# Kernel tuning notes

Measured on AMD Instinct MI355X. Metric: run time of the kernel, lower is better.

The kernel has to match this reference:

```python
import jax, jax.numpy as jnp
import numpy as np

N, IN, OUT, R, E = 20000, 768, 768, 8, 320000


def setup_inputs() -> dict:
    key = jax.random.key(0)
    ks = jax.random.split(key, 9)
    x = jax.random.normal(ks[0], (N, IN), dtype=jnp.float32)
    edge_index = jax.random.randint(ks[1], (2, E), 0, N, dtype=jnp.int64)
    edge_type = jax.random.randint(ks[2], (E,), 0, R, dtype=jnp.int64)
    s1 = 1.0 / np.sqrt(IN)
    s2 = 1.0 / np.sqrt(OUT)
    W1 = jax.random.normal(ks[3], (R, IN, OUT), dtype=jnp.float32) * s1
    root1 = jax.random.normal(ks[4], (IN, OUT), dtype=jnp.float32) * s1
    b1 = jnp.zeros((OUT,), dtype=jnp.float32)
    W2 = jax.random.normal(ks[5], (R, OUT, OUT), dtype=jnp.float32) * s2
    root2 = jax.random.normal(ks[6], (OUT, OUT), dtype=jnp.float32) * s2
    b2 = jnp.zeros((OUT,), dtype=jnp.float32)
    return {"x": x, "edge_index": edge_index, "edge_type": edge_type,
            "W1": W1, "root1": root1, "b1": b1,
            "W2": W2, "root2": root2, "b2": b2}


def _rgcn_conv(x, src, dst, etype, W, root, b):
    # PyG RGCNConv: per-relation mean aggregation of neighbor features,
    # then relation-specific linear transform, plus root weight and bias.
    # mean(x_j @ W_r) == mean(x_j) @ W_r, so aggregate first, transform after.
    num_nodes = x.shape[0]
    num_rel = W.shape[0]
    x_src = x[src]                                  # [E, d_in]
    seg = dst * num_rel + etype                     # composite (node, relation) id
    sums = jax.ops.segment_sum(x_src, seg, num_segments=num_nodes * num_rel)
    cnt = jax.ops.segment_sum(jnp.ones((src.shape[0],), dtype=x.dtype), seg,
                              num_segments=num_nodes * num_rel)
    mean = sums / jnp.maximum(cnt, 1.0)[:, None]    # [N*R, d_in]
    mean = mean.reshape(num_nodes, num_rel, -1)     # [N, R, d_in]
    out = jnp.einsum('nri,rio->no', mean, W)        # relation-batched matmul
    return out + x @ root + b


def reference(x, edge_index, edge_type, W1, root1, b1, W2, root2, b2):
    src, dst = edge_index[0], edge_index[1]
    h = _rgcn_conv(x, src, dst, edge_type, W1, root1, b1)
    h = jax.nn.relu(h)
    out = _rgcn_conv(h, src, dst, edge_type, W2, root2, b2)
    return out
```

## Files before the change

### kernel.cpp

```cpp
#include <hip/hip_runtime.h>
#include <hip/hip_bf16.h>
#include <stdint.h>

#define N_NODES 20000
#define DIM     768
#define NREL    8
#define NEDGE   320000
#define NSEG    (N_NODES * NREL)
#define GKA     6144
#define GK      6912
#define NPW     2

typedef short short8 __attribute__((ext_vector_type(8)));
typedef float f32x4  __attribute__((ext_vector_type(4)));

__device__ __forceinline__ void async_load16(const void* g, void* l) {
  __builtin_amdgcn_global_load_lds((const __attribute__((address_space(1))) void*)g,
                                   (__attribute__((address_space(3))) void*)l,
                                   16, 0, 0);
}

__device__ __forceinline__ float bf_lo(uint32_t v) {
  return __builtin_bit_cast(float, v << 16);
}
__device__ __forceinline__ float bf_hi(uint32_t v) {
  return __builtin_bit_cast(float, v & 0xffff0000u);
}
__device__ __forceinline__ uint32_t pack_bf16x2(float a, float b) {
  uint32_t lo = __builtin_bit_cast(unsigned short, __float2bfloat16(a));
  uint32_t hi = __builtin_bit_cast(unsigned short, __float2bfloat16(b));
  return lo | (hi << 16);
}

__global__ void seg_count_kernel(const int* __restrict__ dst, const int* __restrict__ et,
                                 int* __restrict__ segcnt, int e_cnt) {
  int e = blockIdx.x * 256 + threadIdx.x;
  if (e < e_cnt) atomicAdd(&segcnt[dst[e] * NREL + et[e]], 1);
}

__global__ void block_scan_kernel(const int* __restrict__ in, int* __restrict__ out,
                                  int* __restrict__ partials, int n) {
  __shared__ int wsum[16];
  const int t = threadIdx.x, lane = t & 63, wave = t >> 6;
  const int i = blockIdx.x * 1024 + t;
  int v = (i < n) ? in[i] : 0;
  int s = v;
#pragma unroll
  for (int off = 1; off < 64; off <<= 1) {
    int u = __shfl_up(s, off, 64);
    if (lane >= off) s += u;
  }
  if (lane == 63) wsum[wave] = s;
  __syncthreads();
  if (t < 16) {
    int w = wsum[t];
#pragma unroll
    for (int off = 1; off < 16; off <<= 1) {
      int u = __shfl_up(w, off, 64);
      if (t >= off) w += u;
    }
    wsum[t] = w;
  }
  __syncthreads();
  const int basew = (wave > 0) ? wsum[wave - 1] : 0;
  if (i < n) out[i] = basew + s - v;
  if (t == 1023) partials[blockIdx.x] = wsum[15];
}

__global__ void partial_scan_kernel(int* __restrict__ partials, int nb) {
  const int lane = threadIdx.x & 63;
  int carry = 0;
  for (int base = 0; base < nb; base += 64) {
    const int i = base + lane;
    int v = (i < nb) ? partials[i] : 0;
    int s = v;
#pragma unroll
    for (int off = 1; off < 64; off <<= 1) {
      int u = __shfl_up(s, off, 64);
      if (lane >= off) s += u;
    }
    if (i < nb) partials[i] = carry + s - v;
    carry += __shfl(s, 63, 64);
  }
}

__global__ void add_offsets_kernel(int* __restrict__ soffs, const int* __restrict__ partials,
                                   int* __restrict__ cursor, int n) {
  const int i = blockIdx.x * 1024 + threadIdx.x;
  if (i < n) {
    const int v = soffs[i] + partials[blockIdx.x];
    soffs[i] = v;
    cursor[i] = v;
  }
  if (i == 0) soffs[n] = NEDGE;
}

__global__ void seg_scatter_kernel(const int* __restrict__ src, const int* __restrict__ dst,
                                   const int* __restrict__ et, int* __restrict__ cursor,
                                   int* __restrict__ es, int e_cnt) {
  int e = blockIdx.x * 256 + threadIdx.x;
  if (e < e_cnt) {
    const int seg = dst[e] * NREL + et[e];
    const int p = atomicAdd(&cursor[seg], 1);
    es[p] = src[e];
  }
}

__global__ void cvt_bf16_kernel(const float4* __restrict__ in, ushort4* __restrict__ out, int n4) {
  int i = blockIdx.x * 256 + threadIdx.x;
  if (i < n4) {
    float4 f = in[i];
    ushort4 r;
    r.x = __builtin_bit_cast(unsigned short, __float2bfloat16(f.x));
    r.y = __builtin_bit_cast(unsigned short, __float2bfloat16(f.y));
    r.z = __builtin_bit_cast(unsigned short, __float2bfloat16(f.z));
    r.w = __builtin_bit_cast(unsigned short, __float2bfloat16(f.w));
    out[i] = r;
  }
}

__global__ void transpose_w_kernel(const float* __restrict__ src, __hip_bfloat16* __restrict__ dst,
                                   int rows, int col_off) {
  __shared__ float tile[32][33];
  const int c0 = blockIdx.x * 32;
  const int r0 = blockIdx.y * 32;
  const int tx = threadIdx.x, ty = threadIdx.y;
  for (int i = ty; i < 32; i += 8) {
    int r = r0 + i, c = c0 + tx;
    tile[i][tx] = (r < rows) ? src[(size_t)r * DIM + c] : 0.f;
  }
  __syncthreads();
  for (int i = ty; i < 32; i += 8) {
    int c = c0 + i, r = r0 + tx;
    if (r < rows)
      dst[(size_t)c * GK + col_off + r] = __float2bfloat16(tile[tx][i]);
  }
}

__global__ __launch_bounds__(256) void aggregate_kernel(
    const __hip_bfloat16* __restrict__ feat,
    const int* __restrict__ soffs, const int* __restrict__ es,
    __hip_bfloat16* __restrict__ Abuf,
    int node_base, int rows) {
  const int t = threadIdx.x;
  const int lane = t & 63;
  const int wave = t >> 6;
  const int boff = lane * 8;

  int nloc = (blockIdx.x * 4 + wave) * NPW;
  for (int it = 0; it < NPW; ++it, ++nloc) {
    if (nloc >= rows) return;
    const int n = node_base + nloc;
    char* Ab = (char*)(Abuf + (size_t)nloc * GKA);
#pragma unroll
    for (int r = 0; r < NREL; ++r) {
      const int beg = soffs[n * NREL + r], end = soffs[n * NREL + r + 1];
      float acc[12];
#pragma unroll
      for (int i = 0; i < 12; ++i) acc[i] = 0.f;
      int e = beg;
      for (; e + 2 <= end; e += 2) {
        const int s0 = es[e], s1 = es[e + 1];
        const char* p0 = (const char*)(feat + (size_t)s0 * DIM) + boff;
        const char* p1 = (const char*)(feat + (size_t)s1 * DIM) + boff;
        const uint2 a0 = *(const uint2*)(p0);
        const uint2 a1 = *(const uint2*)(p0 + 512);
        const uint2 a2 = *(const uint2*)(p0 + 1024);
        const uint2 b0 = *(const uint2*)(p1);
        const uint2 b1 = *(const uint2*)(p1 + 512);
        const uint2 b2 = *(const uint2*)(p1 + 1024);
        acc[0]  += bf_lo(a0.x); acc[1]  += bf_hi(a0.x);
        acc[2]  += bf_lo(a0.y); acc[3]  += bf_hi(a0.y);
        acc[4]  += bf_lo(a1.x); acc[5]  += bf_hi(a1.x);
        acc[6]  += bf_lo(a1.y); acc[7]  += bf_hi(a1.y);
        acc[8]  += bf_lo(a2.x); acc[9]  += bf_hi(a2.x);
        acc[10] += bf_lo(a2.y); acc[11] += bf_hi(a2.y);
        acc[0]  += bf_lo(b0.x); acc[1]  += bf_hi(b0.x);
        acc[2]  += bf_lo(b0.y); acc[3]  += bf_hi(b0.y);
        acc[4]  += bf_lo(b1.x); acc[5]  += bf_hi(b1.x);
        acc[6]  += bf_lo(b1.y); acc[7]  += bf_hi(b1.y);
        acc[8]  += bf_lo(b2.x); acc[9]  += bf_hi(b2.x);
        acc[10] += bf_lo(b2.y); acc[11] += bf_hi(b2.y);
      }
      if (e < end) {
        const int s0 = es[e];
        const char* p0 = (const char*)(feat + (size_t)s0 * DIM) + boff;
        const uint2 a0 = *(const uint2*)(p0);
        const uint2 a1 = *(const uint2*)(p0 + 512);
        const uint2 a2 = *(const uint2*)(p0 + 1024);
        acc[0]  += bf_lo(a0.x); acc[1]  += bf_hi(a0.x);
        acc[2]  += bf_lo(a0.y); acc[3]  += bf_hi(a0.y);
        acc[4]  += bf_lo(a1.x); acc[5]  += bf_hi(a1.x);
        acc[6]  += bf_lo(a1.y); acc[7]  += bf_hi(a1.y);
        acc[8]  += bf_lo(a2.x); acc[9]  += bf_hi(a2.x);
        acc[10] += bf_lo(a2.y); acc[11] += bf_hi(a2.y);
      }
      const float inv = 1.f / fmaxf((float)(end - beg), 1.f);
      uint2 o0, o1, o2;
      o0.x = pack_bf16x2(acc[0] * inv, acc[1] * inv);
      o0.y = pack_bf16x2(acc[2] * inv, acc[3] * inv);
      o1.x = pack_bf16x2(acc[4] * inv, acc[5] * inv);
      o1.y = pack_bf16x2(acc[6] * inv, acc[7] * inv);
      o2.x = pack_bf16x2(acc[8] * inv, acc[9] * inv);
      o2.y = pack_bf16x2(acc[10] * inv, acc[11] * inv);
      char* dst = Ab + r * (DIM * 2);
      *(uint2*)(dst + boff) = o0;
      *(uint2*)(dst + boff + 512) = o1;
      *(uint2*)(dst + boff + 1024) = o2;
    }
  }
}

__global__ __launch_bounds__(256, 3) void gemm_kernel(
    const __hip_bfloat16* __restrict__ A,
    const __hip_bfloat16* __restrict__ feat,
    const __hip_bfloat16* __restrict__ BT,
    const float* __restrict__ bias,
    __hip_bfloat16* __restrict__ outb,
    float* __restrict__ outf,
    int mvalid, int node_base, int mode) {
  __shared__ __hip_bfloat16 Asm[128][64];
  __shared__ __hip_bfloat16 Bsm[128][64];
  const int t = threadIdx.x;
  const int lane = t & 63;
  const int wave = t >> 6;
  const int m0 = blockIdx.y * 128;
  const int n0 = blockIdx.x * 128;

  const int srow = lane >> 3;
  const int sg = (lane & 7) ^ srow;
  const int arow = m0 + wave * 32 + srow;
  const __hip_bfloat16* ag = A  + (size_t)arow * GKA + sg * 8;
  const __hip_bfloat16* fg = feat + (size_t)(node_base + arow) * DIM + sg * 8;
  const __hip_bfloat16* bg = BT + (size_t)(n0 + wave * 32 + srow) * GK + sg * 8;

  f32x4 acc[4][4] = {};
  const int wm = (wave >> 1) * 64;
  const int wn = (wave & 1) * 64;
  const int ml = lane & 15;
  const int quad = lane >> 4;
  const int sw = ml & 7;

#define KSTEP(APTR, ASTRIDE)                                                       \
  {                                                                                \
    __syncthreads();                                                               \
    _Pragma("unroll")                                                              \
    for (int ib = 0; ib < 4; ++ib)                                                 \
      async_load16(APTR + (size_t)ib * 8 * (ASTRIDE), &Asm[wave * 32 + ib * 8][0]);\
    _Pragma("unroll")                                                              \
    for (int ib = 0; ib < 4; ++ib)                                                 \
      async_load16(bg + (size_t)ib * 8 * GK, &Bsm[wave * 32 + ib * 8][0]);         \
    bg += 64;                                                                      \
    __syncthreads();                                                               \
    _Pragma("unroll")                                                              \
    for (int ks = 0; ks < 2; ++ks) {                                               \
      const int go = (((ks * 4 + quad) ^ sw) * 8);                                 \
      short8 a[4], b[4];                                                           \
      _Pragma("unroll")                                                            \
      for (int i = 0; i < 4; ++i) a[i] = *(const short8*)&Asm[wm + i * 16 + ml][go];\
      _Pragma("unroll")                                                            \
      for (int i = 0; i < 4; ++i) b[i] = *(const short8*)&Bsm[wn + i * 16 + ml][go];\
      _Pragma("unroll")                                                            \
      for (int i = 0; i < 4; ++i)                                                  \
        _Pragma("unroll")                                                          \
        for (int j = 0; j < 4; ++j)                                                \
          acc[i][j] = __builtin_amdgcn_mfma_f32_16x16x32_bf16(a[i], b[j], acc[i][j], 0, 0, 0); \
    }                                                                              \
  }

  for (int kt = 0; kt < GKA / 64; ++kt) {
    KSTEP(ag, GKA);
    ag += 64;
  }
  for (int kt = 0; kt < DIM / 64; ++kt) {
    KSTEP(fg, DIM);
    fg += 64;
  }
#undef KSTEP

  float bcol[4];
#pragma unroll
  for (int nt = 0; nt < 4; ++nt) bcol[nt] = bias[n0 + wn + nt * 16 + ml];
#pragma unroll
  for (int mt = 0; mt < 4; ++mt) {
#pragma unroll
    for (int rr = 0; rr < 4; ++rr) {
      int row = m0 + wm + mt * 16 + quad * 4 + rr;
      if (row < mvalid) {
        size_t orow = (size_t)(node_base + row) * DIM;
#pragma unroll
        for (int nt = 0; nt < 4; ++nt) {
          int col = n0 + wn + nt * 16 + ml;
          float v = acc[mt][nt][rr] + bcol[nt];
          if (mode == 0) outb[orow + col] = __float2bfloat16(fmaxf(v, 0.f));
          else           outf[orow + col] = v;
        }
      }
    }
  }
}

extern "C" void kernel_launch(void* const* d_in, const int* in_sizes, int n_in,
                              void* d_out, int out_size, void* d_ws, size_t ws_size,
                              hipStream_t stream) {
  const float* x     = (const float*)d_in[0];
  const int*   eidx  = (const int*)d_in[1];
  const int*   etype = (const int*)d_in[2];
  const float* W1    = (const float*)d_in[3];
  const float* root1 = (const float*)d_in[4];
  const float* b1    = (const float*)d_in[5];
  const float* W2    = (const float*)d_in[6];
  const float* root2 = (const float*)d_in[7];
  const float* b2    = (const float*)d_in[8];
  float* out = (float*)d_out;
  const int* esrc_in = eidx;
  const int* edst_in = eidx + NEDGE;

  char* p = (char*)d_ws;
  auto alloc = [&](size_t bytes) -> char* {
    char* r = p;
    p += (bytes + 255) & ~(size_t)255;
    return r;
  };
  __hip_bfloat16* xb  = (__hip_bfloat16*)alloc((size_t)N_NODES * DIM * 2);
  __hip_bfloat16* hb  = (__hip_bfloat16*)alloc((size_t)N_NODES * DIM * 2);
  __hip_bfloat16* w1t = (__hip_bfloat16*)alloc((size_t)DIM * GK * 2);
  __hip_bfloat16* w2t = (__hip_bfloat16*)alloc((size_t)DIM * GK * 2);
  int* segcnt   = (int*)alloc((size_t)NSEG * 4);
  int* soffs    = (int*)alloc((size_t)(NSEG + 1) * 4);
  int* cursor   = (int*)alloc((size_t)NSEG * 4);
  int* partials = (int*)alloc(256 * 4);
  int* es       = (int*)alloc((size_t)NEDGE * 4);
  size_t used = (size_t)(p - (char*)d_ws);
  size_t remain = (ws_size > used) ? (ws_size - used) : 0;
  long long caprows_ll = (long long)(remain / ((size_t)GKA * 2));
  int caprows = (int)((caprows_ll / 128) * 128);
  if (caprows > 20096) caprows = 20096;
  if (caprows < 128) caprows = 128;
  __hip_bfloat16* Abuf = (__hip_bfloat16*)p;

  const int NB = (NSEG + 1023) / 1024;
  hipMemsetAsync(segcnt, 0, (size_t)NSEG * 4, stream);
  seg_count_kernel<<<(NEDGE + 255) / 256, 256, 0, stream>>>(edst_in, etype, segcnt, NEDGE);
  block_scan_kernel<<<NB, 1024, 0, stream>>>(segcnt, soffs, partials, NSEG);
  partial_scan_kernel<<<1, 64, 0, stream>>>(partials, NB);
  add_offsets_kernel<<<NB, 1024, 0, stream>>>(soffs, partials, cursor, NSEG);
  seg_scatter_kernel<<<(NEDGE + 255) / 256, 256, 0, stream>>>(esrc_in, edst_in, etype, cursor, es, NEDGE);

  cvt_bf16_kernel<<<((N_NODES * DIM / 4) + 255) / 256, 256, 0, stream>>>(
      (const float4*)x, (ushort4*)xb, N_NODES * DIM / 4);
  dim3 tb(32, 8);
  transpose_w_kernel<<<dim3(DIM / 32, (NREL * DIM) / 32), tb, 0, stream>>>(W1, w1t, NREL * DIM, 0);
  transpose_w_kernel<<<dim3(DIM / 32, DIM / 32), tb, 0, stream>>>(root1, w1t, DIM, NREL * DIM);
  transpose_w_kernel<<<dim3(DIM / 32, (NREL * DIM) / 32), tb, 0, stream>>>(W2, w2t, NREL * DIM, 0);
  transpose_w_kernel<<<dim3(DIM / 32, DIM / 32), tb, 0, stream>>>(root2, w2t, DIM, NREL * DIM);

  for (int base = 0; base < N_NODES; base += caprows) {
    int rows = N_NODES - base; if (rows > caprows) rows = caprows;
    int agrid = (rows + 4 * NPW - 1) / (4 * NPW);
    aggregate_kernel<<<agrid, 256, 0, stream>>>(xb, soffs, es, Abuf, base, rows);
    dim3 grid(DIM / 128, (rows + 127) / 128);
    gemm_kernel<<<grid, 256, 0, stream>>>(Abuf, xb, w1t, b1, hb, nullptr, rows, base, 0);
  }
  for (int base = 0; base < N_NODES; base += caprows) {
    int rows = N_NODES - base; if (rows > caprows) rows = caprows;
    int agrid = (rows + 4 * NPW - 1) / (4 * NPW);
    aggregate_kernel<<<agrid, 256, 0, stream>>>(hb, soffs, es, Abuf, base, rows);
    dim3 grid(DIM / 128, (rows + 127) / 128);
    gemm_kernel<<<grid, 256, 0, stream>>>(Abuf, hb, w2t, b2, nullptr, out, rows, base, 1);
  }
}
```

Baseline: 1.116 ms.

## Rewrite GEMM as 256x256 tile, 8-wave, double-buffered pipelined kernel with XCD swizzle

The relation-batched GEMM moves from 128x128 tiles with 4 waves and a single LDS buffer to 256x256 tiles with 8 waves. Loads are split into half-tile stages with double buffering, explicit vmcnt/lgkmcnt waits, barriers and setprio, so global-to-LDS loads overlap the MFMA work. Block IDs are remapped so that neighbouring tiles land on the same XCD, and out-of-range rows are clamped instead of loaded past the end. This aims to raise arithmetic intensity and hide memory latency. The cost is a much smaller grid (3 column tiles) and higher register and LDS pressure, which may reduce occupancy.

```diff
diff --git a/kernel.cpp b/kernel.cpp
--- a/kernel.cpp
+++ b/kernel.cpp
@@ -9,6 +9,7 @@
 #define NSEG    (N_NODES * NREL)
 #define GKA     6144
 #define GK      6912
+#define NT_TILES (GK / 64)
 #define NPW     2
 
 typedef short short8 __attribute__((ext_vector_type(8)));
@@ -19,6 +20,8 @@
                                    (__attribute__((address_space(3))) void*)l,
                                    16, 0, 0);
 }
+
+__device__ __forceinline__ int imin(int a, int b) { return a < b ? a : b; }
 
 __device__ __forceinline__ float bf_lo(uint32_t v) {
   return __builtin_bit_cast(float, v << 16);
@@ -211,7 +214,7 @@
   }
 }
 
-__global__ __launch_bounds__(256, 3) void gemm_kernel(
+__global__ __launch_bounds__(512, 2) void gemm_kernel(
     const __hip_bfloat16* __restrict__ A,
     const __hip_bfloat16* __restrict__ feat,
     const __hip_bfloat16* __restrict__ BT,
@@ -219,85 +222,171 @@
     __hip_bfloat16* __restrict__ outb,
     float* __restrict__ outf,
     int mvalid, int node_base, int mode) {
-  __shared__ __hip_bfloat16 Asm[128][64];
-  __shared__ __hip_bfloat16 Bsm[128][64];
+  __shared__ __hip_bfloat16 lds[2][2][2][128][64];
+
   const int t = threadIdx.x;
   const int lane = t & 63;
-  const int wave = t >> 6;
-  const int m0 = blockIdx.y * 128;
-  const int n0 = blockIdx.x * 128;
-
-  const int srow = lane >> 3;
-  const int sg = (lane & 7) ^ srow;
-  const int arow = m0 + wave * 32 + srow;
-  const __hip_bfloat16* ag = A  + (size_t)arow * GKA + sg * 8;
-  const __hip_bfloat16* fg = feat + (size_t)(node_base + arow) * DIM + sg * 8;
-  const __hip_bfloat16* bg = BT + (size_t)(n0 + wave * 32 + srow) * GK + sg * 8;
-
-  f32x4 acc[4][4] = {};
-  const int wm = (wave >> 1) * 64;
-  const int wn = (wave & 1) * 64;
+  const int wid = t >> 6;
+  const int wave_m = wid >> 2;
+  const int wave_n = wid & 3;
   const int ml = lane & 15;
   const int quad = lane >> 4;
-  const int sw = ml & 7;
-
-#define KSTEP(APTR, ASTRIDE)                                                       \
-  {                                                                                \
-    __syncthreads();                                                               \
-    _Pragma("unroll")                                                              \
-    for (int ib = 0; ib < 4; ++ib)                                                 \
-      async_load16(APTR + (size_t)ib * 8 * (ASTRIDE), &Asm[wave * 32 + ib * 8][0]);\
-    _Pragma("unroll")                                                              \
-    for (int ib = 0; ib < 4; ++ib)                                                 \
-      async_load16(bg + (size_t)ib * 8 * GK, &Bsm[wave * 32 + ib * 8][0]);         \
-    bg += 64;                                                                      \
-    __syncthreads();                                                               \
-    _Pragma("unroll")                                                              \
-    for (int ks = 0; ks < 2; ++ks) {                                               \
-      const int go = (((ks * 4 + quad) ^ sw) * 8);                                 \
-      short8 a[4], b[4];                                                           \
-      _Pragma("unroll")                                                            \
-      for (int i = 0; i < 4; ++i) a[i] = *(const short8*)&Asm[wm + i * 16 + ml][go];\
-      _Pragma("unroll")                                                            \
-      for (int i = 0; i < 4; ++i) b[i] = *(const short8*)&Bsm[wn + i * 16 + ml][go];\
-      _Pragma("unroll")                                                            \
-      for (int i = 0; i < 4; ++i)                                                  \
-        _Pragma("unroll")                                                          \
-        for (int j = 0; j < 4; ++j)                                                \
-          acc[i][j] = __builtin_amdgcn_mfma_f32_16x16x32_bf16(a[i], b[j], acc[i][j], 0, 0, 0); \
-    }                                                                              \
-  }
-
-  for (int kt = 0; kt < GKA / 64; ++kt) {
-    KSTEP(ag, GKA);
-    ag += 64;
-  }
-  for (int kt = 0; kt < DIM / 64; ++kt) {
-    KSTEP(fg, DIM);
-    fg += 64;
-  }
-#undef KSTEP
-
-  float bcol[4];
-#pragma unroll
-  for (int nt = 0; nt < 4; ++nt) bcol[nt] = bias[n0 + wn + nt * 16 + ml];
-#pragma unroll
-  for (int mt = 0; mt < 4; ++mt) {
-#pragma unroll
-    for (int rr = 0; rr < 4; ++rr) {
-      int row = m0 + wm + mt * 16 + quad * 4 + rr;
-      if (row < mvalid) {
-        size_t orow = (size_t)(node_base + row) * DIM;
-#pragma unroll
-        for (int nt = 0; nt < 4; ++nt) {
-          int col = n0 + wn + nt * 16 + ml;
-          float v = acc[mt][nt][rr] + bcol[nt];
-          if (mode == 0) outb[orow + col] = __float2bfloat16(fmaxf(v, 0.f));
-          else           outf[orow + col] = v;
+  const int sw8 = ml & 7;
+  const int lsub = lane >> 3;
+  const int lg = (lane & 7) ^ lsub;
+  const int wrow = wid * 8;
+
+  const int nbx = gridDim.x;
+  const int nwg = nbx * gridDim.y;
+  const int lid = blockIdx.y * nbx + blockIdx.x;
+  const int q = nwg >> 3, r = nwg & 7;
+  const int xcd = lid & 7, off = lid >> 3;
+  const int swz = (xcd < r ? xcd * (q + 1) : r * (q + 1) + (xcd - r) * q) + off;
+  const int m0 = (swz / nbx) * 256;
+  const int n0 = (swz % nbx) * 256;
+
+  const char* cA = (const char*)A;
+  const char* cF = (const char*)feat;
+  const char* cB = (const char*)BT;
+  uint32_t offA[2][2], offF[2][2], offB[2][2];
+#pragma unroll
+  for (int h = 0; h < 2; ++h)
+#pragma unroll
+    for (int i = 0; i < 2; ++i) {
+      const int srow = h * 128 + i * 64 + wrow + lsub;
+      const int ar = imin(m0 + srow, mvalid - 1);
+      const int fr = imin(node_base + m0 + srow, N_NODES - 1);
+      offA[h][i] = (uint32_t)ar * (uint32_t)(GKA * 2) + (uint32_t)(lg * 16);
+      offF[h][i] = (uint32_t)fr * (uint32_t)(DIM * 2) + (uint32_t)(lg * 16);
+      offB[h][i] = (uint32_t)(n0 + srow) * (uint32_t)(GK * 2) + (uint32_t)(lg * 16);
+    }
+
+#define VMCNT(N) asm volatile("s_waitcnt vmcnt(" #N ")" ::: "memory")
+#define LGKM0()  asm volatile("s_waitcnt lgkmcnt(0)" ::: "memory")
+#define BAR()    asm volatile("s_barrier" ::: "memory")
+
+#define STAGE_A(BUF, H, TS) do {                                                   \
+    const char* _s0 = ((TS) < 96) ? cA + offA[H][0] + (size_t)(TS) * 128           \
+                                  : cF + offF[H][0] + (size_t)((TS) - 96) * 128;   \
+    const char* _s1 = ((TS) < 96) ? cA + offA[H][1] + (size_t)(TS) * 128           \
+                                  : cF + offF[H][1] + (size_t)((TS) - 96) * 128;   \
+    async_load16(_s0, &lds[BUF][0][H][wrow][0]);                                   \
+    async_load16(_s1, &lds[BUF][0][H][64 + wrow][0]);                              \
+  } while (0)
+
+#define STAGE_B(BUF, H, TS) do {                                                   \
+    async_load16(cB + offB[H][0] + (size_t)(TS) * 128, &lds[BUF][1][H][wrow][0]);  \
+    async_load16(cB + offB[H][1] + (size_t)(TS) * 128, &lds[BUF][1][H][64 + wrow][0]); \
+  } while (0)
+
+#define LOAD_A(BUF, MH)                                                            \
+  _Pragma("unroll") for (int mi = 0; mi < 4; ++mi)                                 \
+  _Pragma("unroll") for (int kk = 0; kk < 2; ++kk)                                 \
+    a[mi][kk] = *(const short8*)&lds[BUF][0][MH][wave_m * 64 + mi * 16 + ml]       \
+                                              [((kk * 4 + quad) ^ sw8) * 8];
+
+#define LOAD_B(BUF, NH, DST)                                                       \
+  _Pragma("unroll") for (int ni = 0; ni < 2; ++ni)                                 \
+  _Pragma("unroll") for (int kk = 0; kk < 2; ++kk)                                 \
+    DST[ni][kk] = *(const short8*)&lds[BUF][1][NH][wave_n * 32 + ni * 16 + ml]     \
+                                                 [((kk * 4 + quad) ^ sw8) * 8];
+
+#define DO_MFMA(MH, NH, BREG)                                                      \
+  _Pragma("unroll") for (int mi = 0; mi < 4; ++mi)                                 \
+  _Pragma("unroll") for (int ni = 0; ni < 2; ++ni) {                               \
+    acc[MH][NH][mi][ni] = __builtin_amdgcn_mfma_f32_16x16x32_bf16(                 \
+        a[mi][0], BREG[ni][0], acc[MH][NH][mi][ni], 0, 0, 0);                      \
+    acc[MH][NH][mi][ni] = __builtin_amdgcn_mfma_f32_16x16x32_bf16(                 \
+        a[mi][1], BREG[ni][1], acc[MH][NH][mi][ni], 0, 0, 0);                      \
+  }
+
+  f32x4 acc[2][2][4][2] = {};
+  short8 a[4][2];
+  short8 b0[2][2], b1[2][2];
+
+  STAGE_A(0, 0, 0);
+  STAGE_B(0, 0, 0);
+  STAGE_A(0, 1, 0);
+  STAGE_B(0, 1, 0);
+  STAGE_A(1, 0, 1);
+  STAGE_B(1, 0, 1);
+  VMCNT(4);
+  BAR();
+
+#pragma unroll 2
+  for (int T = 0; T < NT_TILES; ++T) {
+    const int buf = T & 1;
+    const int ts1 = (T + 1 < NT_TILES) ? T + 1 : NT_TILES - 1;
+    const int ts2 = (T + 2 < NT_TILES) ? T + 2 : NT_TILES - 1;
+    VMCNT(4);
+    LOAD_A(buf, 0);
+    LOAD_B(buf, 0, b0);
+    STAGE_A(buf ^ 1, 1, ts1);
+    STAGE_B(buf ^ 1, 1, ts1);
+    BAR(); LGKM0();
+    __builtin_amdgcn_s_setprio(1);
+    DO_MFMA(0, 0, b0);
+    __builtin_amdgcn_s_setprio(0);
+    BAR();
+    LOAD_B(buf, 1, b1);
+    BAR(); LGKM0();
+    __builtin_amdgcn_s_setprio(1);
+    DO_MFMA(0, 1, b1);
+    __builtin_amdgcn_s_setprio(0);
+    BAR();
+    LOAD_A(buf, 1);
+    STAGE_A(buf, 0, ts2);
+    BAR(); LGKM0();
+    __builtin_amdgcn_s_setprio(1);
+    DO_MFMA(1, 0, b0);
+    __builtin_amdgcn_s_setprio(0);
+    BAR();
+    VMCNT(6);
+    STAGE_B(buf, 0, ts2);
+    BAR(); LGKM0();
+    __builtin_amdgcn_s_setprio(1);
+    DO_MFMA(1, 1, b1);
+    __builtin_amdgcn_s_setprio(0);
+    BAR();
+  }
+  VMCNT(0);
+
+#undef VMCNT
+#undef LGKM0
+#undef BAR
+#undef STAGE_A
+#undef STAGE_B
+#undef LOAD_A
+#undef LOAD_B
+#undef DO_MFMA
+
+  float bcol[2][2];
+#pragma unroll
+  for (int nh = 0; nh < 2; ++nh)
+#pragma unroll
+    for (int ni = 0; ni < 2; ++ni)
+      bcol[nh][ni] = bias[n0 + nh * 128 + wave_n * 32 + ni * 16 + ml];
+
+#pragma unroll
+  for (int mh = 0; mh < 2; ++mh)
+#pragma unroll
+    for (int mi = 0; mi < 4; ++mi)
+#pragma unroll
+      for (int rr = 0; rr < 4; ++rr) {
+        const int row = m0 + mh * 128 + wave_m * 64 + mi * 16 + quad * 4 + rr;
+        if (row < mvalid) {
+          const size_t orow = (size_t)(node_base + row) * DIM;
+#pragma unroll
+          for (int nh = 0; nh < 2; ++nh)
+#pragma unroll
+            for (int ni = 0; ni < 2; ++ni) {
+              const int col = n0 + nh * 128 + wave_n * 32 + ni * 16 + ml;
+              const float v = acc[mh][nh][mi][ni][rr] + bcol[nh][ni];
+              if (mode == 0) outb[orow + col] = __float2bfloat16(fmaxf(v, 0.f));
+              else           outf[orow + col] = v;
+            }
         }
       }
-    }
-  }
 }
 
 extern "C" void kernel_launch(void* const* d_in, const int* in_sizes, int n_in,
@@ -359,14 +448,14 @@
     int rows = N_NODES - base; if (rows > caprows) rows = caprows;
     int agrid = (rows + 4 * NPW - 1) / (4 * NPW);
     aggregate_kernel<<<agrid, 256, 0, stream>>>(xb, soffs, es, Abuf, base, rows);
-    dim3 grid(DIM / 128, (rows + 127) / 128);
-    gemm_kernel<<<grid, 256, 0, stream>>>(Abuf, xb, w1t, b1, hb, nullptr, rows, base, 0);
+    dim3 grid(DIM / 256, (rows + 255) / 256);
+    gemm_kernel<<<grid, 512, 0, stream>>>(Abuf, xb, w1t, b1, hb, nullptr, rows, base, 0);
   }
   for (int base = 0; base < N_NODES; base += caprows) {
     int rows = N_NODES - base; if (rows > caprows) rows = caprows;
     int agrid = (rows + 4 * NPW - 1) / (4 * NPW);
     aggregate_kernel<<<agrid, 256, 0, stream>>>(hb, soffs, es, Abuf, base, rows);
-    dim3 grid(DIM / 128, (rows + 127) / 128);
-    gemm_kernel<<<grid, 256, 0, stream>>>(Abuf, hb, w2t, b2, nullptr, out, rows, base, 1);
-  }
-}
+    dim3 grid(DIM / 256, (rows + 255) / 256);
+    gemm_kernel<<<grid, 512, 0, stream>>>(Abuf, hb, w2t, b2, nullptr, out, rows, base, 1);
+  }
+}
```

After: 1.142 ms. 1.02x slower.
